# Kernel optimization log

Measured on AMD Instinct MI355X. Metric: run time of the kernel, lower is better.

The kernel has to match this reference:

```python
import jax, jax.numpy as jnp
import numpy as np

N = 100000      # nodes
E = 1600000     # edges (avg degree 16)
IN = 128        # input_dim
HID = 32        # hidden_dim per head (layer 1)
HEADS = 2       # heads (layer 1)
OUT = 32        # output_dim (layer 2, heads=1)
NEG_SLOPE = 0.2 # PyG GATConv default leaky relu slope


def setup_inputs() -> dict:
    key = jax.random.key(0)
    ks = jax.random.split(key, 10)
    s = 0.1  # glorot-ish scale
    x = jax.random.normal(ks[0], (N, IN), jnp.float32)
    edge_index = jax.random.randint(ks[1], (2, E), 0, N, dtype=jnp.int64)
    W1 = jax.random.normal(ks[2], (IN, HEADS * HID), jnp.float32) * s
    a1_src = jax.random.normal(ks[3], (HEADS, HID), jnp.float32) * s
    a1_dst = jax.random.normal(ks[4], (HEADS, HID), jnp.float32) * s
    b1 = jnp.zeros((HEADS * HID,), jnp.float32)
    W2 = jax.random.normal(ks[5], (HEADS * HID, OUT), jnp.float32) * s
    a2_src = jax.random.normal(ks[6], (1, OUT), jnp.float32) * s
    a2_dst = jax.random.normal(ks[7], (1, OUT), jnp.float32) * s
    b2 = jnp.zeros((OUT,), jnp.float32)
    return {"x": x, "edge_index": edge_index, "W1": W1, "a1_src": a1_src,
            "a1_dst": a1_dst, "b1": b1, "W2": W2, "a2_src": a2_src,
            "a2_dst": a2_dst, "b2": b2}


def _gat_layer(x, src, dst, W, a_src, a_dst, b, heads, out_ch, concat, n_nodes):
    # linear projection: [N, heads, out_ch]
    h = (x @ W).reshape(n_nodes, heads, out_ch)
    # per-node attention halves: [N, heads]
    alpha_s = jnp.einsum('nhc,hc->nh', h, a_src)
    alpha_d = jnp.einsum('nhc,hc->nh', h, a_dst)
    # per-edge raw score (message x_j = source node, softmax over dst segment)
    e = jax.nn.leaky_relu(alpha_s[src] + alpha_d[dst], NEG_SLOPE)  # [E, heads]
    # segment softmax over incoming edges of each dst node
    m = jax.ops.segment_max(e, dst, num_segments=n_nodes)          # [N, heads]
    m = jax.lax.stop_gradient(m)
    ee = jnp.exp(e - m[dst])
    denom = jax.ops.segment_sum(ee, dst, num_segments=n_nodes)     # [N, heads]
    alpha = ee / (denom[dst] + 1e-16)                              # [E, heads]
    # weighted scatter-add aggregation
    msg = h[src] * alpha[:, :, None]                               # [E, heads, out_ch]
    out = jax.ops.segment_sum(msg, dst, num_segments=n_nodes)      # [N, heads, out_ch]
    if concat:
        out = out.reshape(n_nodes, heads * out_ch)
    else:
        out = out.mean(axis=1)
    return out + b


def reference(x, edge_index, W1, a1_src, a1_dst, b1, W2, a2_src, a2_dst, b2):
    n = x.shape[0]
    # PyG GATConv adds self-loops by default (both layers, same edge set)
    loop = jnp.arange(n, dtype=edge_index.dtype)
    src = jnp.concatenate([edge_index[0], loop])
    dst = jnp.concatenate([edge_index[1], loop])
    h = _gat_layer(x, src, dst, W1, a1_src, a1_dst, b1, HEADS, HID, True, n)
    h = jax.nn.elu(h)
    return _gat_layer(h, src, dst, W2, a2_src, a2_dst, b2, 1, OUT, False, n)
```

## Files before the change

kernel.cpp:

```cpp
#include <hip/hip_runtime.h>
#include <math.h>

#define N_NODES 100000
#define N_EDGES 1600000
#define IN_DIM  128
#define C1      64
#define OUT_DIM 32
#define NEG_SLOPE 0.2f
#define LOG2E 1.44269504f

#define BSHIFT  8
#define BNODES  256
#define NBUCK   ((N_NODES + BNODES - 1) / BNODES)
#define CAP     5120
#define SLOTS   48
#define GC_STRIDE 16
#define G1_BLOCKS ((N_NODES + 127) / 128)

typedef _Float16 half8 __attribute__((ext_vector_type(8)));
typedef float    f32x4 __attribute__((ext_vector_type(4)));

__device__ __forceinline__ float wexp2(float sc) {
    return __builtin_amdgcn_exp2f(fmaxf(sc, NEG_SLOPE * sc));
}


__global__ void zero_k(int4* __restrict__ p, int n4) {
    int i = blockIdx.x * 256 + threadIdx.x;
    if (i < n4) p[i] = make_int4(0, 0, 0, 0);
}

__global__ __launch_bounds__(1024) void binp1_k(const int* __restrict__ ei,
        int* __restrict__ gcur, int* __restrict__ buf) {
    __shared__ int scnt[NBUCK], sbase[NBUCK], soff[NBUCK];
    int t = threadIdx.x;
    if (t < NBUCK) { scnt[t] = 0; soff[t] = 0; }
    __syncthreads();
    int  s[16], bk[16], ld[16];
    bool v[16];
    #pragma unroll
    for (int i = 0; i < 16; ++i) {
        int e = blockIdx.x * 16384 + i * 1024 + t;
        v[i] = e < N_EDGES;
        int ec = v[i] ? e : 0;
        s[i] = ei[ec];
        int d = ei[N_EDGES + ec];
        bk[i] = d >> BSHIFT;
        ld[i] = d & (BNODES - 1);
        if (v[i]) atomicAdd(&scnt[bk[i]], 1);
    }
    __syncthreads();
    if (t < NBUCK) sbase[t] = atomicAdd(&gcur[t * GC_STRIDE], scnt[t]);
    __syncthreads();
    #pragma unroll
    for (int i = 0; i < 16; ++i) {
        if (v[i]) {
            int p = sbase[bk[i]] + atomicAdd(&soff[bk[i]], 1);
            if (p < CAP) buf[bk[i] * CAP + p] = s[i] | (ld[i] << 17);
        }
    }
}

__global__ __launch_bounds__(256) void binp2_k(const int* __restrict__ gcur,
        const int* __restrict__ buf, int* __restrict__ csr, int* __restrict__ deg) {
    __shared__ int4 lcsr4[BNODES * SLOTS / 4];
    __shared__ int  lcnt[BNODES];
    int* lcsr = (int*)lcsr4;
    int b = blockIdx.x, t = threadIdx.x;
    lcnt[t] = 0;
    __syncthreads();
    int cnt = gcur[b * GC_STRIDE];
    if (cnt > CAP) cnt = CAP;
    const int* bb = buf + b * CAP;
    for (int e = t; e < cnt; e += 256) {
        int vv = bb[e];
        int src = vv & 0x1FFFF;
        int l = vv >> 17;
        int slot = atomicAdd(&lcnt[l], 1);
        if (slot < SLOTS) lcsr[l * SLOTS + slot] = src;
    }
    __syncthreads();
    int c = lcnt[t];
    int slot = c < SLOTS ? c : SLOTS - 1;
    lcsr[t * SLOTS + slot] = b * BNODES + t;
    int cd = c + 1;
    deg[b * BNODES + t] = cd < SLOTS ? cd : SLOTS;
    __syncthreads();
    int4* g4 = (int4*)csr + (size_t)b * (BNODES * SLOTS / 4);
    #pragma unroll
    for (int i = 0; i < BNODES * SLOTS / 4 / 256; ++i)
        g4[t + i * 256] = lcsr4[t + i * 256];
}

__global__ void prep_k(const float* __restrict__ W1, const float* __restrict__ W2,
                       _Float16* __restrict__ w1t, _Float16* __restrict__ w2t) {
    int t = blockIdx.x * 256 + threadIdx.x;
    if (t < IN_DIM * C1) {
        int k = t >> 6, n = t & 63;
        w1t[n * IN_DIM + k] = (_Float16)W1[t];
    }
    if (t < C1 * OUT_DIM) {
        int k = t >> 5, n = t & 31;
        w2t[n * C1 + k] = (_Float16)W2[t];
    }
}

__global__ __launch_bounds__(256) void gemm1_k(const float* __restrict__ x,
        const _Float16* __restrict__ w1t, const float* __restrict__ a_s,
        const float* __restrict__ a_d, _Float16* __restrict__ h,
        float* __restrict__ as_o, float* __restrict__ ad_o) {
    __shared__ _Float16 sh[4][32 * 72];
    int t = threadIdx.x;
    int wv = t >> 6, lane = t & 63, m = lane & 15, q = lane >> 4;
    int rbw = blockIdx.x * 128 + wv * 32;
    f32x4 acc[2][4];
    #pragma unroll
    for (int i = 0; i < 2; ++i)
        #pragma unroll
        for (int j = 0; j < 4; ++j) acc[i][j] = (f32x4){0.f, 0.f, 0.f, 0.f};
    #pragma unroll
    for (int ks = 0; ks < 4; ++ks) {
        half8 a[2];
        #pragma unroll
        for (int rt = 0; rt < 2; ++rt) {
            int r = rbw + rt * 16 + m;
            r = r < N_NODES ? r : 0;
            const float4* p = (const float4*)(x + (size_t)r * IN_DIM + ks * 32 + q * 8);
            float4 f0 = p[0], f1 = p[1];
            half8 av;
            av[0] = (_Float16)f0.x; av[1] = (_Float16)f0.y;
            av[2] = (_Float16)f0.z; av[3] = (_Float16)f0.w;
            av[4] = (_Float16)f1.x; av[5] = (_Float16)f1.y;
            av[6] = (_Float16)f1.z; av[7] = (_Float16)f1.w;
            a[rt] = av;
        }
        #pragma unroll
        for (int ct = 0; ct < 4; ++ct) {
            half8 b = *(const half8*)(w1t + (ct * 16 + m) * IN_DIM + ks * 32 + q * 8);
            acc[0][ct] = __builtin_amdgcn_mfma_f32_16x16x32_f16(a[0], b, acc[0][ct], 0, 0, 0);
            acc[1][ct] = __builtin_amdgcn_mfma_f32_16x16x32_f16(a[1], b, acc[1][ct], 0, 0, 0);
        }
    }
    _Float16* ws = sh[wv];
    #pragma unroll
    for (int rt = 0; rt < 2; ++rt)
        #pragma unroll
        for (int ct = 0; ct < 4; ++ct)
            #pragma unroll
            for (int r = 0; r < 4; ++r)
                ws[(rt * 16 + q * 4 + r) * 72 + ct * 16 + m] = (_Float16)acc[rt][ct][r];
    __syncthreads();
    int rl = lane >> 1, hp = lane & 1;
    int rg = rbw + rl;
    if (rg < N_NODES) {
        float As_r[32], Ad_r[32];
        const float4* ap = (const float4*)(a_s + hp * 32);
        const float4* dp = (const float4*)(a_d + hp * 32);
        #pragma unroll
        for (int i = 0; i < 8; ++i) {
            float4 v = ap[i];
            As_r[4*i] = v.x; As_r[4*i+1] = v.y; As_r[4*i+2] = v.z; As_r[4*i+3] = v.w;
            float4 u = dp[i];
            Ad_r[4*i] = u.x; Ad_r[4*i+1] = u.y; Ad_r[4*i+2] = u.z; Ad_r[4*i+3] = u.w;
        }
        const _Float16* rowp = ws + rl * 72 + hp * 32;
        half8 c0 = *(const half8*)(rowp);
        half8 c1 = *(const half8*)(rowp + 8);
        half8 c2 = *(const half8*)(rowp + 16);
        half8 c3 = *(const half8*)(rowp + 24);
        float s = 0.f, dd = 0.f;
        #pragma unroll
        for (int j = 0; j < 8; ++j) {
            s  = fmaf((float)c0[j], As_r[j],      s);
            dd = fmaf((float)c0[j], Ad_r[j],      dd);
            s  = fmaf((float)c1[j], As_r[8 + j],  s);
            dd = fmaf((float)c1[j], Ad_r[8 + j],  dd);
            s  = fmaf((float)c2[j], As_r[16 + j], s);
            dd = fmaf((float)c2[j], Ad_r[16 + j], dd);
            s  = fmaf((float)c3[j], As_r[24 + j], s);
            dd = fmaf((float)c3[j], Ad_r[24 + j], dd);
        }
        as_o[rg * 2 + hp] = s  * LOG2E;
        ad_o[rg * 2 + hp] = dd * LOG2E;
        _Float16* hr = h + (size_t)rg * C1 + hp * 32;
        *(half8*)(hr)      = c0;
        *(half8*)(hr + 8)  = c1;
        *(half8*)(hr + 16) = c2;
        *(half8*)(hr + 24) = c3;
    }
}

__global__ __launch_bounds__(256) void agg1g2_k(const int* __restrict__ deg,
        const int* __restrict__ csr, const _Float16* __restrict__ h1,
        const float* __restrict__ as1, const float* __restrict__ ad1,
        const float* __restrict__ b1, const _Float16* __restrict__ w2t,
        const float* __restrict__ a2s, const float* __restrict__ a2d,
        _Float16* __restrict__ h2, float* __restrict__ as2o,
        float* __restrict__ ad2o) {
    __shared__ _Float16 shu[16 * 72];
    __shared__ _Float16 sh2[16 * 36];
    int t = threadIdx.x;
    int wv = t >> 6, lane = t & 63;
    int dl   = lane >> 4;
    int eg   = (lane >> 3) & 1;
    int cl   = lane & 7;
    int head = cl >> 2;
    int lr   = wv * 4 + dl;
    int d    = blockIdx.x * 16 + lr;

    int cnt = deg[d];
    const int* row = csr + d * SLOTS;
    float advl = ad1[d * 2 + head];
    float acc[8] = {0.f, 0.f, 0.f, 0.f, 0.f, 0.f, 0.f, 0.f};
    float wsum = 0.f;
    for (int base = 0; base < cnt; base += 8) {
        int e0 = base + eg, e1 = e0 + 2, e2 = e0 + 4, e3 = e0 + 6;
        bool v0 = e0 < cnt, v1 = e1 < cnt, v2 = e2 < cnt, v3 = e3 < cnt;
        int s0 = row[v0 ? e0 : 0];
        int s1 = row[v1 ? e1 : 0];
        int s2 = row[v2 ? e2 : 0];
        int s3 = row[v3 ? e3 : 0];
        float a0 = as1[(unsigned)(s0 * 2 + head)];
        float a1 = as1[(unsigned)(s1 * 2 + head)];
        float a2 = as1[(unsigned)(s2 * 2 + head)];
        float a3 = as1[(unsigned)(s3 * 2 + head)];
        half8 g0 = *(const half8*)(h1 + (unsigned)(s0 * C1 + 8 * cl));
        half8 g1 = *(const half8*)(h1 + (unsigned)(s1 * C1 + 8 * cl));
        half8 g2 = *(const half8*)(h1 + (unsigned)(s2 * C1 + 8 * cl));
        half8 g3 = *(const half8*)(h1 + (unsigned)(s3 * C1 + 8 * cl));
        float w0 = v0 ? wexp2(a0 + advl) : 0.f;
        float w1 = v1 ? wexp2(a1 + advl) : 0.f;
        float w2 = v2 ? wexp2(a2 + advl) : 0.f;
        float w3 = v3 ? wexp2(a3 + advl) : 0.f;
        #pragma unroll
        for (int i = 0; i < 8; ++i) {
            acc[i] = fmaf((float)g0[i], w0, acc[i]);
            acc[i] = fmaf((float)g1[i], w1, acc[i]);
            acc[i] = fmaf((float)g2[i], w2, acc[i]);
            acc[i] = fmaf((float)g3[i], w3, acc[i]);
        }
        wsum += (w0 + w1) + (w2 + w3);
    }
    #pragma unroll
    for (int i = 0; i < 8; ++i) acc[i] += __shfl_xor(acc[i], 8);
    wsum += __shfl_xor(wsum, 8);
    if (eg == 0) {
        float inv = 1.f / (wsum + 1e-16f);
        const float4* bv = (const float4*)(b1 + 8 * cl);
        float o[8];
        #pragma unroll
        for (int i = 0; i < 4; ++i) {
            o[i]     = acc[i]     * inv + (&bv[0].x)[i];
            o[4 + i] = acc[4 + i] * inv + (&bv[1].x)[i];
        }
        half8 hv;
        #pragma unroll
        for (int i = 0; i < 8; ++i) {
            float e = o[i] > 0.f ? o[i] : __expf(o[i]) - 1.f;
            hv[i] = (_Float16)e;
        }
        *(half8*)(shu + lr * 72 + cl * 8) = hv;
    }
    __syncthreads();
    if (wv != 0) return;

    {
        int m = lane & 15, q = lane >> 4;
        f32x4 c2[2];
        c2[0] = (f32x4){0.f, 0.f, 0.f, 0.f};
        c2[1] = (f32x4){0.f, 0.f, 0.f, 0.f};
        #pragma unroll
        for (int ks = 0; ks < 2; ++ks) {
            half8 a = *(const half8*)(shu + m * 72 + ks * 32 + q * 8);
            #pragma unroll
            for (int ct = 0; ct < 2; ++ct) {
                half8 b = *(const half8*)(w2t + (ct * 16 + m) * C1 + ks * 32 + q * 8);
                c2[ct] = __builtin_amdgcn_mfma_f32_16x16x32_f16(a, b, c2[ct], 0, 0, 0);
            }
        }
        #pragma unroll
        for (int ct = 0; ct < 2; ++ct)
            #pragma unroll
            for (int r = 0; r < 4; ++r)
                sh2[(q * 4 + r) * 36 + ct * 16 + m] = (_Float16)c2[ct][r];
    }
    asm volatile("s_waitcnt lgkmcnt(0)" ::: "memory");

    {
        int r = lane & 15, p = lane >> 4;
        int rg = blockIdx.x * 16 + r;
        const float4* ap = (const float4*)(a2s + p * 8);
        const float4* dp = (const float4*)(a2d + p * 8);
        float4 av0 = ap[0], av1 = ap[1];
        float4 dv0 = dp[0], dv1 = dp[1];
        float As[8] = {av0.x, av0.y, av0.z, av0.w, av1.x, av1.y, av1.z, av1.w};
        float Ad[8] = {dv0.x, dv0.y, dv0.z, dv0.w, dv1.x, dv1.y, dv1.z, dv1.w};
        half8 c = *(const half8*)(sh2 + r * 36 + p * 8);
        float s = 0.f, dd = 0.f;
        #pragma unroll
        for (int j = 0; j < 8; ++j) {
            s  = fmaf((float)c[j], As[j], s);
            dd = fmaf((float)c[j], Ad[j], dd);
        }
        s  += __shfl_xor(s, 16);  s  += __shfl_xor(s, 32);
        dd += __shfl_xor(dd, 16); dd += __shfl_xor(dd, 32);
        if (p == 0) {
            as2o[rg] = s  * LOG2E;
            ad2o[rg] = dd * LOG2E;
        }
        *(half8*)(h2 + (size_t)rg * OUT_DIM + p * 8) = c;
    }
}

__global__ __launch_bounds__(256) void agg2_k(const int* __restrict__ deg,
        const int* __restrict__ csr, const _Float16* __restrict__ h2,
        const float* __restrict__ as2, const float* __restrict__ ad2,
        const float* __restrict__ b2, float* __restrict__ out) {
    int lane = threadIdx.x & 63;
    int dl   = lane >> 3;
    int eg   = (lane >> 2) & 1;
    int cl   = lane & 3;
    int d = ((blockIdx.x * 256 + threadIdx.x) >> 6) * 8 + dl;
    int cnt = deg[d];
    const int* row = csr + d * SLOTS;
    float advl = ad2[d];
    float acc[8] = {0.f, 0.f, 0.f, 0.f, 0.f, 0.f, 0.f, 0.f};
    float wsum = 0.f;
    for (int base = 0; base < cnt; base += 8) {
        int e0 = base + eg, e1 = e0 + 2, e2 = e0 + 4, e3 = e0 + 6;
        bool v0 = e0 < cnt, v1 = e1 < cnt, v2 = e2 < cnt, v3 = e3 < cnt;
        int s0 = row[v0 ? e0 : 0];
        int s1 = row[v1 ? e1 : 0];
        int s2 = row[v2 ? e2 : 0];
        int s3 = row[v3 ? e3 : 0];
        float a0 = as2[(unsigned)s0];
        float a1 = as2[(unsigned)s1];
        float a2 = as2[(unsigned)s2];
        float a3 = as2[(unsigned)s3];
        half8 g0 = *(const half8*)(h2 + (unsigned)(s0 * OUT_DIM + 8 * cl));
        half8 g1 = *(const half8*)(h2 + (unsigned)(s1 * OUT_DIM + 8 * cl));
        half8 g2 = *(const half8*)(h2 + (unsigned)(s2 * OUT_DIM + 8 * cl));
        half8 g3 = *(const half8*)(h2 + (unsigned)(s3 * OUT_DIM + 8 * cl));
        float w0 = v0 ? wexp2(a0 + advl) : 0.f;
        float w1 = v1 ? wexp2(a1 + advl) : 0.f;
        float w2 = v2 ? wexp2(a2 + advl) : 0.f;
        float w3 = v3 ? wexp2(a3 + advl) : 0.f;
        #pragma unroll
        for (int i = 0; i < 8; ++i) {
            acc[i] = fmaf((float)g0[i], w0, acc[i]);
            acc[i] = fmaf((float)g1[i], w1, acc[i]);
            acc[i] = fmaf((float)g2[i], w2, acc[i]);
            acc[i] = fmaf((float)g3[i], w3, acc[i]);
        }
        wsum += (w0 + w1) + (w2 + w3);
    }
    #pragma unroll
    for (int i = 0; i < 8; ++i) acc[i] += __shfl_xor(acc[i], 4);
    wsum += __shfl_xor(wsum, 4);
    if (eg == 0) {
        float inv = 1.f / (wsum + 1e-16f);
        const float4* bv = (const float4*)(b2 + 8 * cl);
        float4 o0, o1;
        o0.x = acc[0] * inv + bv[0].x; o0.y = acc[1] * inv + bv[0].y;
        o0.z = acc[2] * inv + bv[0].z; o0.w = acc[3] * inv + bv[0].w;
        o1.x = acc[4] * inv + bv[1].x; o1.y = acc[5] * inv + bv[1].y;
        o1.z = acc[6] * inv + bv[1].z; o1.w = acc[7] * inv + bv[1].w;
        float4* ow = (float4*)(out + (size_t)d * OUT_DIM + 8 * cl);
        ow[0] = o0;
        ow[1] = o1;
    }
}


extern "C" void kernel_launch(void* const* d_in, const int* in_sizes, int n_in,
                              void* d_out, int out_size, void* d_ws, size_t ws_size,
                              hipStream_t stream) {
    const float* x   = (const float*)d_in[0];
    const int*   ei  = (const int*)d_in[1];
    const float* W1  = (const float*)d_in[2];
    const float* a1s = (const float*)d_in[3];
    const float* a1d = (const float*)d_in[4];
    const float* b1  = (const float*)d_in[5];
    const float* W2  = (const float*)d_in[6];
    const float* a2s = (const float*)d_in[7];
    const float* a2d = (const float*)d_in[8];
    const float* b2  = (const float*)d_in[9];
    float* out = (float*)d_out;

    char* ws = (char*)d_ws;
    size_t off = 0;
    auto alloc = [&](size_t bytes) -> void* {
        void* p = ws + off;
        off = (off + bytes + 255) & ~(size_t)255;
        return p;
    };
    int* gcur      = (int*)alloc((size_t)NBUCK * GC_STRIDE * 4);
    int* buf       = (int*)alloc((size_t)NBUCK * CAP * 4);
    int* csr       = (int*)alloc((size_t)NBUCK * BNODES * SLOTS * 4);
    int* deg       = (int*)alloc((size_t)NBUCK * BNODES * 4);
    _Float16* w1t  = (_Float16*)alloc((size_t)IN_DIM * C1 * 2);
    _Float16* w2t  = (_Float16*)alloc((size_t)C1 * OUT_DIM * 2);
    _Float16* h1   = (_Float16*)alloc((size_t)N_NODES * C1 * 2);
    float* as1     = (float*)alloc((size_t)N_NODES * 2 * 4);
    float* ad1     = (float*)alloc((size_t)N_NODES * 2 * 4);
    _Float16* h2   = (_Float16*)alloc((size_t)N_NODES * OUT_DIM * 2);
    float* as2     = (float*)alloc((size_t)N_NODES * 4);
    float* ad2     = (float*)alloc((size_t)N_NODES * 4);

    const int ZN4 = NBUCK * GC_STRIDE / 4;
    zero_k<<<(ZN4 + 255) / 256, 256, 0, stream>>>((int4*)gcur, ZN4);
    binp1_k<<<(N_EDGES + 16383) / 16384, 1024, 0, stream>>>(ei, gcur, buf);
    binp2_k<<<NBUCK, 256, 0, stream>>>(gcur, buf, csr, deg);
    prep_k<<<(IN_DIM * C1 + 255) / 256, 256, 0, stream>>>(W1, W2, w1t, w2t);

    gemm1_k<<<G1_BLOCKS, 256, 0, stream>>>(x, w1t, a1s, a1d, h1, as1, ad1);
    agg1g2_k<<<N_NODES / 16, 256, 0, stream>>>(deg, csr, h1, as1, ad1, b1,
                                               w2t, a2s, a2d, h2, as2, ad2);
    agg2_k<<<N_NODES / 32, 256, 0, stream>>>(deg, csr, h2, as2, ad2, b2, out);
}
```

Measured before the change: 217.6 us.

## Software-pipeline gather loops in aggregation kernels and fold zeroing into prep

Both aggregation kernels now prefetch the next batch of neighbor indices, attention scores and feature vectors into registers while the current batch is weighted and accumulated, so more gather latency is hidden behind arithmetic. Separately, the zero_k launch is removed: prep_k clears the bucket counters and is moved ahead of the binning kernels, saving one kernel launch. The cost is higher register pressure from the double-buffered batches, which could lower occupancy.

```diff
diff --git a/kernel.cpp b/kernel.cpp
--- a/kernel.cpp
+++ b/kernel.cpp
@@ -24,11 +24,6 @@
     return __builtin_amdgcn_exp2f(fmaxf(sc, NEG_SLOPE * sc));
 }
 
-
-__global__ void zero_k(int4* __restrict__ p, int n4) {
-    int i = blockIdx.x * 256 + threadIdx.x;
-    if (i < n4) p[i] = make_int4(0, 0, 0, 0);
-}
 
 __global__ __launch_bounds__(1024) void binp1_k(const int* __restrict__ ei,
         int* __restrict__ gcur, int* __restrict__ buf) {
@@ -93,8 +88,10 @@
 }
 
 __global__ void prep_k(const float* __restrict__ W1, const float* __restrict__ W2,
-                       _Float16* __restrict__ w1t, _Float16* __restrict__ w2t) {
+                       _Float16* __restrict__ w1t, _Float16* __restrict__ w2t,
+                       int* __restrict__ gcur) {
     int t = blockIdx.x * 256 + threadIdx.x;
+    if (t < NBUCK * GC_STRIDE) gcur[t] = 0;
     if (t < IN_DIM * C1) {
         int k = t >> 6, n = t & 63;
         w1t[n * IN_DIM + k] = (_Float16)W1[t];
@@ -213,33 +210,42 @@
     float advl = ad1[d * 2 + head];
     float acc[8] = {0.f, 0.f, 0.f, 0.f, 0.f, 0.f, 0.f, 0.f};
     float wsum = 0.f;
-    for (int base = 0; base < cnt; base += 8) {
-        int e0 = base + eg, e1 = e0 + 2, e2 = e0 + 4, e3 = e0 + 6;
-        bool v0 = e0 < cnt, v1 = e1 < cnt, v2 = e2 < cnt, v3 = e3 < cnt;
-        int s0 = row[v0 ? e0 : 0];
-        int s1 = row[v1 ? e1 : 0];
-        int s2 = row[v2 ? e2 : 0];
-        int s3 = row[v3 ? e3 : 0];
-        float a0 = as1[(unsigned)(s0 * 2 + head)];
-        float a1 = as1[(unsigned)(s1 * 2 + head)];
-        float a2 = as1[(unsigned)(s2 * 2 + head)];
-        float a3 = as1[(unsigned)(s3 * 2 + head)];
-        half8 g0 = *(const half8*)(h1 + (unsigned)(s0 * C1 + 8 * cl));
-        half8 g1 = *(const half8*)(h1 + (unsigned)(s1 * C1 + 8 * cl));
-        half8 g2 = *(const half8*)(h1 + (unsigned)(s2 * C1 + 8 * cl));
-        half8 g3 = *(const half8*)(h1 + (unsigned)(s3 * C1 + 8 * cl));
-        float w0 = v0 ? wexp2(a0 + advl) : 0.f;
-        float w1 = v1 ? wexp2(a1 + advl) : 0.f;
-        float w2 = v2 ? wexp2(a2 + advl) : 0.f;
-        float w3 = v3 ? wexp2(a3 + advl) : 0.f;
-        #pragma unroll
-        for (int i = 0; i < 8; ++i) {
-            acc[i] = fmaf((float)g0[i], w0, acc[i]);
-            acc[i] = fmaf((float)g1[i], w1, acc[i]);
-            acc[i] = fmaf((float)g2[i], w2, acc[i]);
-            acc[i] = fmaf((float)g3[i], w3, acc[i]);
-        }
-        wsum += (w0 + w1) + (w2 + w3);
+
+    float aA[4]; half8 gA[4]; bool vA[4];
+    #pragma unroll
+    for (int i = 0; i < 4; ++i) {
+        int e = eg + 2 * i;
+        vA[i] = e < cnt;
+        int s = row[vA[i] ? e : 0];
+        aA[i] = as1[(unsigned)(s * 2 + head)];
+        gA[i] = *(const half8*)(h1 + (unsigned)(s * C1 + 8 * cl));
+    }
+    for (int base = 0;;) {
+        int nb = base + 8;
+        bool more = nb < cnt;
+        float aB[4]; half8 gB[4]; bool vB[4];
+        if (more) {
+            #pragma unroll
+            for (int i = 0; i < 4; ++i) {
+                int e = nb + eg + 2 * i;
+                vB[i] = e < cnt;
+                int s = row[vB[i] ? e : 0];
+                aB[i] = as1[(unsigned)(s * 2 + head)];
+                gB[i] = *(const half8*)(h1 + (unsigned)(s * C1 + 8 * cl));
+            }
+        }
+        #pragma unroll
+        for (int i = 0; i < 4; ++i) {
+            float w = vA[i] ? wexp2(aA[i] + advl) : 0.f;
+            wsum += w;
+            #pragma unroll
+            for (int j = 0; j < 8; ++j)
+                acc[j] = fmaf((float)gA[i][j], w, acc[j]);
+        }
+        if (!more) break;
+        base = nb;
+        #pragma unroll
+        for (int i = 0; i < 4; ++i) { aA[i] = aB[i]; gA[i] = gB[i]; vA[i] = vB[i]; }
     }
     #pragma unroll
     for (int i = 0; i < 8; ++i) acc[i] += __shfl_xor(acc[i], 8);
@@ -326,33 +332,42 @@
     float advl = ad2[d];
     float acc[8] = {0.f, 0.f, 0.f, 0.f, 0.f, 0.f, 0.f, 0.f};
     float wsum = 0.f;
-    for (int base = 0; base < cnt; base += 8) {
-        int e0 = base + eg, e1 = e0 + 2, e2 = e0 + 4, e3 = e0 + 6;
-        bool v0 = e0 < cnt, v1 = e1 < cnt, v2 = e2 < cnt, v3 = e3 < cnt;
-        int s0 = row[v0 ? e0 : 0];
-        int s1 = row[v1 ? e1 : 0];
-        int s2 = row[v2 ? e2 : 0];
-        int s3 = row[v3 ? e3 : 0];
-        float a0 = as2[(unsigned)s0];
-        float a1 = as2[(unsigned)s1];
-        float a2 = as2[(unsigned)s2];
-        float a3 = as2[(unsigned)s3];
-        half8 g0 = *(const half8*)(h2 + (unsigned)(s0 * OUT_DIM + 8 * cl));
-        half8 g1 = *(const half8*)(h2 + (unsigned)(s1 * OUT_DIM + 8 * cl));
-        half8 g2 = *(const half8*)(h2 + (unsigned)(s2 * OUT_DIM + 8 * cl));
-        half8 g3 = *(const half8*)(h2 + (unsigned)(s3 * OUT_DIM + 8 * cl));
-        float w0 = v0 ? wexp2(a0 + advl) : 0.f;
-        float w1 = v1 ? wexp2(a1 + advl) : 0.f;
-        float w2 = v2 ? wexp2(a2 + advl) : 0.f;
-        float w3 = v3 ? wexp2(a3 + advl) : 0.f;
-        #pragma unroll
-        for (int i = 0; i < 8; ++i) {
-            acc[i] = fmaf((float)g0[i], w0, acc[i]);
-            acc[i] = fmaf((float)g1[i], w1, acc[i]);
-            acc[i] = fmaf((float)g2[i], w2, acc[i]);
-            acc[i] = fmaf((float)g3[i], w3, acc[i]);
-        }
-        wsum += (w0 + w1) + (w2 + w3);
+
+    float aA[4]; half8 gA[4]; bool vA[4];
+    #pragma unroll
+    for (int i = 0; i < 4; ++i) {
+        int e = eg + 2 * i;
+        vA[i] = e < cnt;
+        int s = row[vA[i] ? e : 0];
+        aA[i] = as2[(unsigned)s];
+        gA[i] = *(const half8*)(h2 + (unsigned)(s * OUT_DIM + 8 * cl));
+    }
+    for (int base = 0;;) {
+        int nb = base + 8;
+        bool more = nb < cnt;
+        float aB[4]; half8 gB[4]; bool vB[4];
+        if (more) {
+            #pragma unroll
+            for (int i = 0; i < 4; ++i) {
+                int e = nb + eg + 2 * i;
+                vB[i] = e < cnt;
+                int s = row[vB[i] ? e : 0];
+                aB[i] = as2[(unsigned)s];
+                gB[i] = *(const half8*)(h2 + (unsigned)(s * OUT_DIM + 8 * cl));
+            }
+        }
+        #pragma unroll
+        for (int i = 0; i < 4; ++i) {
+            float w = vA[i] ? wexp2(aA[i] + advl) : 0.f;
+            wsum += w;
+            #pragma unroll
+            for (int j = 0; j < 8; ++j)
+                acc[j] = fmaf((float)gA[i][j], w, acc[j]);
+        }
+        if (!more) break;
+        base = nb;
+        #pragma unroll
+        for (int i = 0; i < 4; ++i) { aA[i] = aB[i]; gA[i] = gB[i]; vA[i] = vB[i]; }
     }
     #pragma unroll
     for (int i = 0; i < 8; ++i) acc[i] += __shfl_xor(acc[i], 4);
@@ -407,11 +422,9 @@
     float* as2     = (float*)alloc((size_t)N_NODES * 4);
     float* ad2     = (float*)alloc((size_t)N_NODES * 4);
 
-    const int ZN4 = NBUCK * GC_STRIDE / 4;
-    zero_k<<<(ZN4 + 255) / 256, 256, 0, stream>>>((int4*)gcur, ZN4);
+    prep_k<<<(IN_DIM * C1 + 255) / 256, 256, 0, stream>>>(W1, W2, w1t, w2t, gcur);
     binp1_k<<<(N_EDGES + 16383) / 16384, 1024, 0, stream>>>(ei, gcur, buf);
     binp2_k<<<NBUCK, 256, 0, stream>>>(gcur, buf, csr, deg);
-    prep_k<<<(IN_DIM * C1 + 255) / 256, 256, 0, stream>>>(W1, W2, w1t, w2t);
 
     gemm1_k<<<G1_BLOCKS, 256, 0, stream>>>(x, w1t, a1s, a1d, h1, as1, ad1);
     agg1g2_k<<<N_NODES / 16, 256, 0, stream>>>(deg, csr, h1, as1, ad1, b1,
```

Measured after the change: 229.6 us. +5.5%, slower.
